# Performance work log

Measured on AMD Instinct MI355X. Metric: run time of the kernel, lower is better.

The kernel has to match this reference:

```python
import jax, jax.numpy as jnp
import numpy as np

B, Q, KL, ML, D = 2, 1024, 1024, 1024, 1024
H, DK = 16, 64  # adim = H*DK = 1024
SCALE = float(np.sqrt(DK))


def _rel_shift(x):
    # x: [B, qlen, klen, H] -> TransformerXL relative shift
    b, q, k, h = x.shape
    x = jnp.pad(x, ((0, 0), (0, 0), (1, 0), (0, 0)))  # [B,q,k+1,H]
    x = x.reshape(b, k + 1, q, h)[:, 1:]               # drop first row of shifted view
    return x.reshape(b, q, k, h)


def setup_inputs() -> dict:
    key = jax.random.key(0)
    ks = jax.random.split(key, 12)
    n = lambda i, s, scale=1.0: jax.random.normal(ks[i], s, jnp.float32) * scale
    return {
        "key_x": n(0, (B, KL, D)),
        "query": n(1, (B, Q, D)),
        "memory": n(2, (B, ML, D)),
        "pos_embs": n(3, (KL + ML, 1, D)),
        "mask": jnp.ones((B, Q, KL + ML), jnp.int32),
        "u": n(4, (H, DK), 0.02),
        "v": n(5, (H, DK), 0.02),
        "w_key": n(6, (D, H * DK), 0.02),
        "w_value": n(7, (D, H * DK), 0.02),
        "w_query": n(8, (D, H * DK), 0.02),
        "w_position": n(9, (D, H * DK), 0.02),
        "w_out": n(10, (H * DK, D), 0.02),
    }


def reference(key_x, query, memory, pos_embs, mask, u, v,
              w_key, w_value, w_query, w_position, w_out):
    bs, qlen = query.shape[:2]
    kv = jnp.concatenate([memory, key_x], axis=1)          # [B, mlen+klen, D]
    klen_tot = kv.shape[1]
    val = (kv @ w_value).reshape(bs, klen_tot, H, DK)
    k = (kv @ w_key).reshape(bs, klen_tot, H, DK)
    q = (query @ w_query).reshape(bs, qlen, H, DK)
    pos = (pos_embs.reshape(-1, pos_embs.shape[-1]) @ w_position).reshape(-1, H, DK)
    AC = jnp.einsum('bihd,bjhd->bijh', q + u[None, None], k)
    BD = jnp.einsum('bihd,jhd->bijh', q + v[None, None], pos)
    BD = _rel_shift(BD)
    e = (AC + BD) / SCALE                                   # [B, q, k, H]
    neg_inf = jnp.finfo(e.dtype).min
    e = jnp.where(mask[..., None] == 0, neg_inf, e)
    aw = jax.nn.softmax(e, axis=2)
    cv = jnp.einsum('bijh,bjhd->bihd', aw, val).reshape(bs, qlen, H * DK)
    cv = cv @ w_out
    return cv, aw.transpose(0, 3, 1, 2)
```

## Files before the change

### kernel.cpp

```cpp
#include <hip/hip_runtime.h>
#include <stdint.h>

#define H 16
#define DK 64
#define QL 1024
#define KT 2048
#define DM 1024
#define BATCH 2

typedef __attribute__((ext_vector_type(4))) float f32x4;
typedef __attribute__((ext_vector_type(8))) short s16x8;

enum { EPI_K = 0, EPI_V = 1, EPI_QUV = 2, EPI_P = 3, EPI_OUT = 4 };

__device__ __forceinline__ unsigned short f2bf(float f) {
  union { float f; uint32_t u; } v; v.f = f;
  uint32_t u = v.u;
  u += 0x7fffu + ((u >> 16) & 1u);
  return (unsigned short)(u >> 16);
}

#define MFMA_BF16(A, B, C) __builtin_amdgcn_mfma_f32_16x16x32_bf16((A), (B), (C), 0, 0, 0)

__device__ __forceinline__ void gld_lds16(const void* g, void* l) {
  __builtin_amdgcn_global_load_lds(
      (const __attribute__((address_space(1))) void*)g,
      (__attribute__((address_space(3))) void*)l, 16, 0, 0);
}

__device__ __forceinline__ void store_bf16_col(char* base, int g, int col2, const f32x4& v) {
  uint32_t pk01, pk23;
  asm("v_cvt_pk_bf16_f32 %0, %1, %2" : "=v"(pk01) : "v"(v[0]), "v"(v[1]));
  asm("v_cvt_pk_bf16_f32 %0, %1, %2" : "=v"(pk23) : "v"(v[2]), "v"(v[3]));
  const int rr = g * 4;
  *(uint16_t*)(base + (rr + 0) * 128 + (col2 ^ (((rr + 0) & 7) << 4))) = (uint16_t)pk01;
  *(uint16_t*)(base + (rr + 1) * 128 + (col2 ^ (((rr + 1) & 7) << 4))) = (uint16_t)(pk01 >> 16);
  *(uint16_t*)(base + (rr + 2) * 128 + (col2 ^ (((rr + 2) & 7) << 4))) = (uint16_t)pk23;
  *(uint16_t*)(base + (rr + 3) * 128 + (col2 ^ (((rr + 3) & 7) << 4))) = (uint16_t)(pk23 >> 16);
}


__global__ __launch_bounds__(256) void cast_kv_kernel(
    const float* __restrict__ mem, const float* __restrict__ keyx,
    unsigned short* __restrict__ kv) {
  size_t i4 = (size_t)blockIdx.x * blockDim.x + threadIdx.x;
  if (i4 >= (size_t)BATCH * KT * DM / 4) return;
  size_t e = i4 * 4;
  int b = (int)(e >> 21);
  int rem = (int)(e & ((1u << 21) - 1));
  int j = rem >> 10;
  int d = rem & 1023;
  const float* src = (j < 1024)
      ? (mem + ((size_t)b << 20) + ((size_t)j << 10) + d)
      : (keyx + ((size_t)b << 20) + ((size_t)(j - 1024) << 10) + d);
  float4 v = *(const float4*)src;
  ushort4 o;
  o.x = f2bf(v.x); o.y = f2bf(v.y); o.z = f2bf(v.z); o.w = f2bf(v.w);
  *(ushort4*)(kv + e) = o;
}

__global__ __launch_bounds__(256) void cast4_kernel(
    const float* __restrict__ src, unsigned short* __restrict__ dst, int n4) {
  int i4 = blockIdx.x * blockDim.x + threadIdx.x;
  if (i4 >= n4) return;
  float4 v = *(const float4*)(src + (size_t)i4 * 4);
  ushort4 o;
  o.x = f2bf(v.x); o.y = f2bf(v.y); o.z = f2bf(v.z); o.w = f2bf(v.w);
  *(ushort4*)(dst + (size_t)i4 * 4) = o;
}

__global__ __launch_bounds__(256) void transpose_cast_kernel(
    const float* __restrict__ w0, const float* __restrict__ w1,
    const float* __restrict__ w2, const float* __restrict__ w3,
    const float* __restrict__ w4,
    unsigned short* __restrict__ o0, unsigned short* __restrict__ o1,
    unsigned short* __restrict__ o2, unsigned short* __restrict__ o3,
    unsigned short* __restrict__ o4) {
  __shared__ float tile[32][33];
  const float* src; unsigned short* dst;
  switch (blockIdx.z) {
    case 0: src = w0; dst = o0; break;
    case 1: src = w1; dst = o1; break;
    case 2: src = w2; dst = o2; break;
    case 3: src = w3; dst = o3; break;
    default: src = w4; dst = o4; break;
  }
  int bx = blockIdx.x * 32, by = blockIdx.y * 32;
  int tx = threadIdx.x;
  int ty = threadIdx.y;
#pragma unroll
  for (int r = 0; r < 4; ++r)
    tile[ty + r * 8][tx] = src[(size_t)(by + ty + r * 8) * DM + bx + tx];
  __syncthreads();
#pragma unroll
  for (int r = 0; r < 4; ++r)
    dst[(size_t)(bx + ty + r * 8) * DM + by + tx] = f2bf(tile[tx][ty + r * 8]);
}

__global__ __launch_bounds__(256) void pack_mask_kernel(
    const int* __restrict__ mask, unsigned long long* __restrict__ bits) {
  int t = blockIdx.x * blockDim.x + threadIdx.x;
  int wid = t >> 6, lane = t & 63;
  int v = mask[(size_t)wid * 64 + lane];
  unsigned long long bb = __ballot(v != 0);
  if (lane == 0) bits[wid] = bb;
}


__device__ __forceinline__ void gemm_body(
    const unsigned short* __restrict__ A, const unsigned short* __restrict__ B,
    int mode,
    unsigned short* __restrict__ out0, unsigned short* __restrict__ out1,
    float* __restrict__ outf,
    const float* __restrict__ uvec, const float* __restrict__ vvec,
    int bx, int by) {
  __shared__ __align__(16) unsigned short lds[128 * 64 * 2];
  char* As = (char*)lds;
  char* Bs = (char*)lds + 128 * 64 * 2;

  const int tid = threadIdx.x;
  const int w = tid >> 6, lane = tid & 63;
  const int g = lane >> 4, l15 = lane & 15;
  const int m0 = by * 128, n0 = bx * 128;
  const int wm = w >> 1, wn = w & 1;
  const int K = 1024;

  f32x4 zf = {0.f, 0.f, 0.f, 0.f};
  f32x4 acc[4][4];
#pragma unroll
  for (int a = 0; a < 4; ++a)
#pragma unroll
    for (int c = 0; c < 4; ++c) acc[a][c] = zf;

  for (int kt = 0; kt < K; kt += 64) {
#pragma unroll
    for (int q = 0; q < 4; ++q) {
      int o = (w * 4 + q) * 1024 + lane * 16;
      int row = o >> 7;
      int slot = (o & 127) >> 4;
      int ks = slot ^ (row & 7);
      gld_lds16(A + (size_t)(m0 + row) * K + kt + ks * 8, As + o);
      gld_lds16(B + (size_t)(n0 + row) * K + kt + ks * 8, Bs + o);
    }
    asm volatile("s_waitcnt vmcnt(0)" ::: "memory");
    __syncthreads();
#pragma unroll
    for (int kk = 0; kk < 2; ++kk) {
      s16x8 af[4], bfr[4];
#pragma unroll
      for (int mf = 0; mf < 4; ++mf) {
        int row = wm * 64 + mf * 16 + l15;
        af[mf] = *(const s16x8*)(As + row * 128 + ((kk * 64 + g * 16) ^ ((row & 7) << 4)));
      }
#pragma unroll
      for (int nf = 0; nf < 4; ++nf) {
        int row = wn * 64 + nf * 16 + l15;
        bfr[nf] = *(const s16x8*)(Bs + row * 128 + ((kk * 64 + g * 16) ^ ((row & 7) << 4)));
      }
#pragma unroll
      for (int mf = 0; mf < 4; ++mf)
#pragma unroll
        for (int nf = 0; nf < 4; ++nf)
          acc[mf][nf] = MFMA_BF16(af[mf], bfr[nf], acc[mf][nf]);
    }
    __syncthreads();
  }

#pragma unroll
  for (int mf = 0; mf < 4; ++mf) {
#pragma unroll
    for (int nf = 0; nf < 4; ++nf) {
#pragma unroll
      for (int i = 0; i < 4; ++i) {
        int m = m0 + wm * 64 + mf * 16 + g * 4 + i;
        int n = n0 + wn * 64 + nf * 16 + l15;
        float val = acc[mf][nf][i];
        if (mode == EPI_K) {
          int b = m >> 11, j = m & 2047, hh = n >> 6, d = n & 63;
          out0[(((size_t)(b * H + hh) * KT + j) << 6) + d] = f2bf(val);
        } else if (mode == EPI_V) {
          int hh = m >> 6, d = m & 63, b = n >> 11, j = n & 2047;
          out0[((size_t)(b * H + hh) * 64 + d) * KT + j] = f2bf(val);
        } else if (mode == EPI_QUV) {
          int b = m >> 10, i2 = m & 1023, hh = n >> 6, d = n & 63;
          size_t idx = ((size_t)(b * H + hh) * QL + i2) * 64 + d;
          out0[idx] = f2bf(val + uvec[n]);
          out1[idx] = f2bf(val + vvec[n]);
        } else if (mode == EPI_P) {
          int hh = n >> 6, d = n & 63;
          out0[(((size_t)hh * KT + m) << 6) + d] = f2bf(val);
        } else {
          outf[(size_t)m * DM + n] = val;
        }
      }
    }
  }
}

__global__ __launch_bounds__(256) void gemm_fused_kernel(
    const unsigned short* __restrict__ kv, const unsigned short* __restrict__ q_b,
    const unsigned short* __restrict__ pos_b,
    const unsigned short* __restrict__ wk, const unsigned short* __restrict__ wv,
    const unsigned short* __restrict__ wq, const unsigned short* __restrict__ wp,
    unsigned short* __restrict__ Kp, unsigned short* __restrict__ Vt,
    unsigned short* __restrict__ Qu, unsigned short* __restrict__ Qv,
    unsigned short* __restrict__ Pp,
    const float* __restrict__ u, const float* __restrict__ v) {
  int bid = blockIdx.x;
  const unsigned short *A, *B;
  unsigned short *o0, *o1 = nullptr;
  int mode, bx, by;
  if (bid < 256)      { A = kv;    B = wk; mode = EPI_K;   o0 = Kp; bx = bid & 7;  by = bid >> 3; }
  else if (bid < 512) { bid -= 256; A = wv; B = kv; mode = EPI_V;   o0 = Vt; bx = bid & 31; by = bid >> 5; }
  else if (bid < 640) { bid -= 512; A = q_b; B = wq; mode = EPI_QUV; o0 = Qu; o1 = Qv; bx = bid & 7; by = bid >> 3; }
  else                { bid -= 640; A = pos_b; B = wp; mode = EPI_P; o0 = Pp; bx = bid & 7; by = bid >> 3; }
  gemm_body(A, B, mode, o0, o1, nullptr, u, v, bx, by);
}

__global__ __launch_bounds__(256) void gemm_out_kernel(
    const unsigned short* __restrict__ A, const unsigned short* __restrict__ B,
    float* __restrict__ outf) {
  gemm_body(A, B, EPI_OUT, nullptr, nullptr, outf, nullptr, nullptr, blockIdx.x, blockIdx.y);
}


__device__ __forceinline__ void bd_chunk(
    f32x4 (&out)[4], const unsigned short* __restrict__ Pp_b,
    const s16x8* qv, const s16x8* qvp, int tbase, int g, int l15) {
  const s16x8 zv = {0, 0, 0, 0, 0, 0, 0, 0};
  const f32x4 zf = {0.f, 0.f, 0.f, 0.f};
#pragma unroll
  for (int nf = 0; nf < 4; ++nf) {
    const int F0 = tbase + nf * 16;
    const bool wrap = (F0 >= KT);
    const int prow = (wrap ? F0 - (KT + 1) : F0) + l15;
    const s16x8* psrc = (const s16x8*)(Pp_b + (size_t)(prow < 0 ? 0 : prow) * 64 + g * 8);
    f32x4 c = zf;
#pragma unroll
    for (int kk = 0; kk < 2; ++kk) {
      s16x8 pb = psrc[kk * 4];
      if (prow < 0) pb = zv;
      c = MFMA_BF16(wrap ? qvp[kk] : qv[kk], pb, c);
    }
    out[nf] = c;
  }
}

__device__ __forceinline__ void bd_gather(
    float (&bd)[4][4], const f32x4 (&cur)[4], const f32x4& nxt0,
    const int (&slan)[4], const bool (&crr)[4]) {
#pragma unroll
  for (int i = 0; i < 4; ++i) {
    float s0 = __shfl(cur[0][i], slan[i]);
    float s1 = __shfl(cur[1][i], slan[i]);
    float s2 = __shfl(cur[2][i], slan[i]);
    float s3 = __shfl(cur[3][i], slan[i]);
    float s4 = __shfl(nxt0[i], slan[i]);
    bd[0][i] = crr[i] ? s1 : s0;
    bd[1][i] = crr[i] ? s2 : s1;
    bd[2][i] = crr[i] ? s3 : s2;
    bd[3][i] = crr[i] ? s4 : s3;
  }
}

__device__ __forceinline__ void load_k(
    s16x8 (&kb)[2][4], const unsigned short* __restrict__ Kp_b,
    int j0, int g, int l15) {
#pragma unroll
  for (int nf = 0; nf < 4; ++nf) {
    const s16x8* p = (const s16x8*)(Kp_b + (size_t)(j0 + nf * 16 + l15) * 64 + g * 8);
    kb[0][nf] = p[0];
    kb[1][nf] = p[4];
  }
}

__device__ __forceinline__ void load_v(
    s16x8 (&vb)[2][4], const unsigned short* __restrict__ Vt_b,
    int j0, int g, int l15) {
#pragma unroll
  for (int df = 0; df < 4; ++df) {
    const unsigned short* p = Vt_b + (size_t)(df * 16 + l15) * KT + j0 + g * 8;
    vb[0][df] = *(const s16x8*)(p);
    vb[1][df] = *(const s16x8*)(p + 32);
  }
}

__device__ __forceinline__ void qk_acc(
    f32x4 (&acc)[4], const s16x8* qu, const s16x8 (&kb)[2][4]) {
#pragma unroll
  for (int kk = 0; kk < 2; ++kk)
#pragma unroll
    for (int nf = 0; nf < 4; ++nf)
      acc[nf] = MFMA_BF16(qu[kk], kb[kk][nf], acc[nf]);
}

__device__ __forceinline__ void make_e(
    float (&e)[4][4], const f32x4 (&acc)[4], const float (&bd)[4][4],
    const unsigned long long* __restrict__ mb_b,
    int r0, int s, int g, int l15) {
#pragma unroll
  for (int i = 0; i < 4; ++i) {
    unsigned long long mw = mb_b[(size_t)(r0 + g * 4 + i) * 32 + s];
#pragma unroll
    for (int nf = 0; nf < 4; ++nf) {
      float ev = (acc[nf][i] + bd[nf][i]) * 0.125f;
      e[nf][i] = ((mw >> (nf * 16 + l15)) & 1ull) ? ev : -1e30f;
    }
  }
}

#define ATTN_DECODE()                                                  \
  const int w = threadIdx.x >> 6, lane = threadIdx.x & 63;             \
  const int g = lane >> 4, l15 = lane & 15;                            \
  const int logical = ((blockIdx.x & 7) << 9) | (blockIdx.x >> 3);     \
  const int rblk = logical & 15, jq = (logical >> 4) & 7, bh = logical >> 7; \
  const int b = bh >> 4, h = bh & 15;                                  \
  const int r0 = rblk * 64 + w * 16;                                   \
  (void)b; (void)h;

#define ATTN_PROLOGUE()                                                \
  s16x8 zv = {0, 0, 0, 0, 0, 0, 0, 0};                                 \
  s16x8 qu[2], qv[2], qvp[2];                                          \
  {                                                                    \
    int r = r0 + l15;                                                  \
    const s16x8* pq = (const s16x8*)(Qu_b + (size_t)r * 64 + g * 8);   \
    const s16x8* pv = (const s16x8*)(Qv_b + (size_t)r * 64 + g * 8);   \
    qu[0] = pq[0]; qu[1] = pq[4];                                      \
    qv[0] = pv[0]; qv[1] = pv[4];                                      \
    int rp = r0 + 1 + l15;                                             \
    if (rp < QL) {                                                     \
      const s16x8* pp = (const s16x8*)(Qv_b + (size_t)rp * 64 + g * 8);\
      qvp[0] = pp[0]; qvp[1] = pp[4];                                  \
    } else { qvp[0] = zv; qvp[1] = zv; }                               \
  }                                                                    \
  int slan[4]; bool crr[4];                                            \
  _Pragma("unroll")                                                    \
  for (int i = 0; i < 4; ++i) {                                        \
    int g4i = g * 4 + i;                                               \
    slan[i] = (lane & 48) | ((l15 + 15 - g4i) & 15);                   \
    crr[i] = (l15 >= g4i + 1);                                         \
  }                                                                    \
  const int sq0 = jq * 4;                                              \
  const int tb0 = sq0 * 64 + 1008 - r0;

__global__ __launch_bounds__(256) void attn_p1(
    const unsigned short* __restrict__ Qu, const unsigned short* __restrict__ Qv,
    const unsigned short* __restrict__ Kp, const unsigned short* __restrict__ Pp,
    const unsigned long long* __restrict__ mbits,
    float2* __restrict__ mlp, float* __restrict__ Oacc) {
  ATTN_DECODE();

  if (jq == 0) {
    float4 z4 = {0.f, 0.f, 0.f, 0.f};
    float* dst = Oacc + ((size_t)bh * QL + rblk * 64) * 64 + threadIdx.x * 16;
#pragma unroll
    for (int q = 0; q < 4; ++q) ((float4*)dst)[q] = z4;
  }

  const unsigned short* Qu_b = Qu + (size_t)bh * QL * 64;
  const unsigned short* Qv_b = Qv + (size_t)bh * QL * 64;
  const unsigned short* Kp_b = Kp + (size_t)bh * KT * 64;
  const unsigned short* Pp_b = Pp + (size_t)h * KT * 64;
  const unsigned long long* mb_b = mbits + (size_t)b * QL * 32;

  ATTN_PROLOGUE();

  float m_l[4], l_l[4];
#pragma unroll
  for (int i = 0; i < 4; ++i) { m_l[i] = -1e30f; l_l[i] = 0.f; }

  f32x4 cur[4], nxt[4];
  bd_chunk(cur, Pp_b, qv, qvp, tb0, g, l15);
  s16x8 kb[2][4];
  load_k(kb, Kp_b, sq0 * 64, g, l15);

#pragma unroll
  for (int ss = 0; ss < 4; ++ss) {
    const int s = sq0 + ss;
    bd_chunk(nxt, Pp_b, qv, qvp, tb0 + (ss + 1) * 64, g, l15);
    f32x4 acc[4];
#pragma unroll
    for (int nf = 0; nf < 4; ++nf) acc[nf] = f32x4{0.f, 0.f, 0.f, 0.f};
    qk_acc(acc, qu, kb);
    if (ss < 3) load_k(kb, Kp_b, (s + 1) * 64, g, l15);
    float bd[4][4];
    bd_gather(bd, cur, nxt[0], slan, crr);
    float e[4][4];
    make_e(e, acc, bd, mb_b, r0, s, g, l15);
#pragma unroll
    for (int i = 0; i < 4; ++i) {
      float tmax = fmaxf(fmaxf(e[0][i], e[1][i]), fmaxf(e[2][i], e[3][i]));
      float mnew = fmaxf(m_l[i], tmax);
      l_l[i] = l_l[i] * __expf(m_l[i] - mnew) + __expf(e[0][i] - mnew) +
               __expf(e[1][i] - mnew) + __expf(e[2][i] - mnew) + __expf(e[3][i] - mnew);
      m_l[i] = mnew;
    }
#pragma unroll
    for (int nf = 0; nf < 4; ++nf) cur[nf] = nxt[nf];
  }

#pragma unroll
  for (int i = 0; i < 4; ++i) {
    float m_r = m_l[i];
#pragma unroll
    for (int d = 1; d < 16; d <<= 1) m_r = fmaxf(m_r, __shfl_xor(m_r, d));
    float contrib = l_l[i] * __expf(m_l[i] - m_r);
#pragma unroll
    for (int d = 1; d < 16; d <<= 1) contrib += __shfl_xor(contrib, d);
    if (l15 == 0) {
      float2 p2; p2.x = m_r; p2.y = contrib;
      mlp[((size_t)bh * QL + r0 + g * 4 + i) * 8 + jq] = p2;
    }
  }
}

__global__ __launch_bounds__(256) void attn_p2(
    const unsigned short* __restrict__ Qu, const unsigned short* __restrict__ Qv,
    const unsigned short* __restrict__ Kp, const unsigned short* __restrict__ Vt,
    const unsigned short* __restrict__ Pp,
    const unsigned long long* __restrict__ mbits,
    const float2* __restrict__ mlp,
    float* __restrict__ aw, float* __restrict__ Oacc) {
  __shared__ __align__(16) unsigned short smem[8192];
  ATTN_DECODE();

  const unsigned short* Qu_b = Qu + (size_t)bh * QL * 64;
  const unsigned short* Qv_b = Qv + (size_t)bh * QL * 64;
  const unsigned short* Kp_b = Kp + (size_t)bh * KT * 64;
  const unsigned short* Vt_b = Vt + (size_t)bh * 64 * KT;
  const unsigned short* Pp_b = Pp + (size_t)h * KT * 64;
  float* aw_b = aw + (size_t)bh * QL * KT;
  const unsigned long long* mb_b = mbits + (size_t)b * QL * 32;
  char* pl0 = (char*)smem + w * 4096;
  char* pl1 = pl0 + 2048;

  float m_f = -1e30f, l_f = 0.f;
  {
    float2 mq[8];
#pragma unroll
    for (int q = 0; q < 8; ++q) mq[q] = mlp[((size_t)bh * QL + r0 + l15) * 8 + q];
#pragma unroll
    for (int q = 0; q < 8; ++q) m_f = fmaxf(m_f, mq[q].x);
#pragma unroll
    for (int q = 0; q < 8; ++q) l_f += mq[q].y * __expf(mq[q].x - m_f);
  }
  float rl = 1.f / l_f;
  float m_fi[4], rl_i[4];
#pragma unroll
  for (int i = 0; i < 4; ++i) {
    m_fi[i] = __shfl(m_f, g * 4 + i);
    rl_i[i] = __shfl(rl, g * 4 + i);
  }

  ATTN_PROLOGUE();

  f32x4 accO[4];
#pragma unroll
  for (int df = 0; df < 4; ++df) accO[df] = f32x4{0.f, 0.f, 0.f, 0.f};

  f32x4 cur[4], nxt[4];
  bd_chunk(cur, Pp_b, qv, qvp, tb0, g, l15);
  s16x8 kb[2][4], vb[2][4];
  load_k(kb, Kp_b, sq0 * 64, g, l15);

#pragma unroll
  for (int ss = 0; ss < 4; ++ss) {
    const int s = sq0 + ss;
    const int j0 = s * 64;
    bd_chunk(nxt, Pp_b, qv, qvp, tb0 + (ss + 1) * 64, g, l15);
    f32x4 acc[4];
#pragma unroll
    for (int nf = 0; nf < 4; ++nf) acc[nf] = f32x4{0.f, 0.f, 0.f, 0.f};
    qk_acc(acc, qu, kb);
    if (ss < 3) load_k(kb, Kp_b, j0 + 64, g, l15);
    float bd[4][4];
    bd_gather(bd, cur, nxt[0], slan, crr);
    float e[4][4];
    make_e(e, acc, bd, mb_b, r0, s, g, l15);

    if (ss > 0) {
      char* prd = (ss & 1) ? pl0 : pl1;
#pragma unroll
      for (int kk = 0; kk < 2; ++kk) {
        s16x8 pa = *(const s16x8*)(prd + l15 * 128 + ((kk * 64 + g * 16) ^ ((l15 & 7) << 4)));
#pragma unroll
        for (int df = 0; df < 4; ++df)
          accO[df] = MFMA_BF16(pa, vb[kk][df], accO[df]);
      }
    }
    load_v(vb, Vt_b, j0, g, l15);

    char* pwr = (ss & 1) ? pl1 : pl0;
#pragma unroll
    for (int nf = 0; nf < 4; ++nf) {
      f32x4 pv4;
#pragma unroll
      for (int i = 0; i < 4; ++i) {
        float p = __expf(e[nf][i] - m_fi[i]) * rl_i[i];
        aw_b[(size_t)(r0 + g * 4 + i) * KT + j0 + nf * 16 + l15] = p;
        pv4[i] = p;
      }
      store_bf16_col(pwr, g, (nf * 16 + l15) * 2, pv4);
    }
#pragma unroll
    for (int nf = 0; nf < 4; ++nf) cur[nf] = nxt[nf];
  }

  {
#pragma unroll
    for (int kk = 0; kk < 2; ++kk) {
      s16x8 pa = *(const s16x8*)(pl1 + l15 * 128 + ((kk * 64 + g * 16) ^ ((l15 & 7) << 4)));
#pragma unroll
      for (int df = 0; df < 4; ++df)
        accO[df] = MFMA_BF16(pa, vb[kk][df], accO[df]);
    }
  }

#pragma unroll
  for (int df = 0; df < 4; ++df)
#pragma unroll
    for (int i = 0; i < 4; ++i)
      atomicAdd(&Oacc[((size_t)bh * QL + r0 + g * 4 + i) * 64 + df * 16 + l15], accO[df][i]);
}

__global__ __launch_bounds__(256) void cast_cv_kernel(
    const float* __restrict__ Oacc, unsigned short* __restrict__ cvb) {
  int t = blockIdx.x * blockDim.x + threadIdx.x;
  int d4 = t & 15, r = (t >> 4) & 1023, bh = t >> 14;
  int b = bh >> 4, h = bh & 15;
  float4 v = ((const float4*)Oacc)[t];
  ushort4 o;
  o.x = f2bf(v.x); o.y = f2bf(v.y); o.z = f2bf(v.z); o.w = f2bf(v.w);
  *(ushort4*)(cvb + (size_t)(b * QL + r) * DM + h * 64 + d4 * 4) = o;
}


extern "C" void kernel_launch(void* const* d_in, const int* in_sizes, int n_in,
                              void* d_out, int out_size, void* d_ws, size_t ws_size,
                              hipStream_t stream) {
  const float* key_x  = (const float*)d_in[0];
  const float* query  = (const float*)d_in[1];
  const float* memory = (const float*)d_in[2];
  const float* pose   = (const float*)d_in[3];
  const int*   mask   = (const int*)d_in[4];
  const float* u      = (const float*)d_in[5];
  const float* v      = (const float*)d_in[6];
  const float* w_key  = (const float*)d_in[7];
  const float* w_val  = (const float*)d_in[8];
  const float* w_qry  = (const float*)d_in[9];
  const float* w_pos  = (const float*)d_in[10];
  const float* w_out  = (const float*)d_in[11];

  char* ws = (char*)d_ws;
  const size_t MB = 1024 * 1024;
  unsigned short* kv_b  = (unsigned short*)(ws + 0);
  unsigned short* q_b   = (unsigned short*)(ws + 8 * MB);
  unsigned short* pos_b = (unsigned short*)(ws + 12 * MB);
  unsigned short* wk_t  = (unsigned short*)(ws + 16 * MB);
  unsigned short* wv_t  = (unsigned short*)(ws + 18 * MB);
  unsigned short* wq_t  = (unsigned short*)(ws + 20 * MB);
  unsigned short* wp_t  = (unsigned short*)(ws + 22 * MB);
  unsigned short* wo_t  = (unsigned short*)(ws + 24 * MB);
  unsigned short* Kp    = (unsigned short*)(ws + 26 * MB);
  unsigned short* Vt    = (unsigned short*)(ws + 34 * MB);
  unsigned short* Qu    = (unsigned short*)(ws + 42 * MB);
  unsigned short* Qv    = (unsigned short*)(ws + 46 * MB);
  unsigned short* Pp    = (unsigned short*)(ws + 50 * MB);
  unsigned short* cvb   = (unsigned short*)(ws + 54 * MB);
  unsigned long long* mb = (unsigned long long*)(ws + 58 * MB);
  float*  Oacc = (float*)(ws + 0);
  float2* mlp  = (float2*)(ws + 8 * MB);

  float* out_cv = (float*)d_out;
  float* out_aw = (float*)d_out + (size_t)BATCH * QL * DM;

  cast_kv_kernel<<<4096, 256, 0, stream>>>(memory, key_x, kv_b);
  cast4_kernel<<<2048, 256, 0, stream>>>(query, q_b, BATCH * QL * DM / 4);
  cast4_kernel<<<2048, 256, 0, stream>>>(pose, pos_b, KT * DM / 4);
  transpose_cast_kernel<<<dim3(32, 32, 5), dim3(32, 8), 0, stream>>>(
      w_key, w_val, w_qry, w_pos, w_out, wk_t, wv_t, wq_t, wp_t, wo_t);
  pack_mask_kernel<<<16384, 256, 0, stream>>>(mask, mb);

  gemm_fused_kernel<<<768, 256, 0, stream>>>(kv_b, q_b, pos_b, wk_t, wv_t, wq_t, wp_t,
                                             Kp, Vt, Qu, Qv, Pp, u, v);

  attn_p1<<<4096, 256, 0, stream>>>(Qu, Qv, Kp, Pp, mb, mlp, Oacc);
  attn_p2<<<4096, 256, 0, stream>>>(Qu, Qv, Kp, Vt, Pp, mb, mlp, out_aw, Oacc);
  cast_cv_kernel<<<2048, 256, 0, stream>>>(Oacc, cvb);

  gemm_out_kernel<<<dim3(8, 16), 256, 0, stream>>>(cvb, wo_t, out_cv);
}
```

Baseline: 483.7 us.

## Store unnormalized softmax in pass one and normalize during a PV-only pass

The first attention pass now computes exp(e) directly, with no running-max subtraction, writes it into the attention-weight output, and records per-chunk row sums. A small kernel turns those sums into reciprocals. A new PV kernel then reads the stored weights back, rescales them in place, converts them to bf16 and runs the PV MFMAs. This removes the second recomputation of the QK and relative-position (BD) scores and the LDS staging. In exchange it adds a full extra read and write of the large fp32 attention-weight tensor. Dropping the max subtraction also risks exp overflow when logits are large.

Measured after the change: 481.5 us. Within noise of the previous version (-0.5%).

```diff
diff --git a/kernel.cpp b/kernel.cpp
--- a/kernel.cpp
+++ b/kernel.cpp
@@ -28,15 +28,13 @@
       (__attribute__((address_space(3))) void*)l, 16, 0, 0);
 }
 
-__device__ __forceinline__ void store_bf16_col(char* base, int g, int col2, const f32x4& v) {
-  uint32_t pk01, pk23;
-  asm("v_cvt_pk_bf16_f32 %0, %1, %2" : "=v"(pk01) : "v"(v[0]), "v"(v[1]));
-  asm("v_cvt_pk_bf16_f32 %0, %1, %2" : "=v"(pk23) : "v"(v[2]), "v"(v[3]));
-  const int rr = g * 4;
-  *(uint16_t*)(base + (rr + 0) * 128 + (col2 ^ (((rr + 0) & 7) << 4))) = (uint16_t)pk01;
-  *(uint16_t*)(base + (rr + 1) * 128 + (col2 ^ (((rr + 1) & 7) << 4))) = (uint16_t)(pk01 >> 16);
-  *(uint16_t*)(base + (rr + 2) * 128 + (col2 ^ (((rr + 2) & 7) << 4))) = (uint16_t)pk23;
-  *(uint16_t*)(base + (rr + 3) * 128 + (col2 ^ (((rr + 3) & 7) << 4))) = (uint16_t)(pk23 >> 16);
+__device__ __forceinline__ s16x8 cvt8(const f32x4& a, const f32x4& b) {
+  union { uint32_t u[4]; s16x8 v; } r;
+  asm("v_cvt_pk_bf16_f32 %0, %1, %2" : "=v"(r.u[0]) : "v"(a[0]), "v"(a[1]));
+  asm("v_cvt_pk_bf16_f32 %0, %1, %2" : "=v"(r.u[1]) : "v"(a[2]), "v"(a[3]));
+  asm("v_cvt_pk_bf16_f32 %0, %1, %2" : "=v"(r.u[2]) : "v"(b[0]), "v"(b[1]));
+  asm("v_cvt_pk_bf16_f32 %0, %1, %2" : "=v"(r.u[3]) : "v"(b[2]), "v"(b[3]));
+  return r.v;
 }
 
 
@@ -316,7 +314,7 @@
   const int rblk = logical & 15, jq = (logical >> 4) & 7, bh = logical >> 7; \
   const int b = bh >> 4, h = bh & 15;                                  \
   const int r0 = rblk * 64 + w * 16;                                   \
-  (void)b; (void)h;
+  (void)b; (void)h; (void)lane;
 
 #define ATTN_PROLOGUE()                                                \
   s16x8 zv = {0, 0, 0, 0, 0, 0, 0, 0};                                 \
@@ -347,7 +345,7 @@
     const unsigned short* __restrict__ Qu, const unsigned short* __restrict__ Qv,
     const unsigned short* __restrict__ Kp, const unsigned short* __restrict__ Pp,
     const unsigned long long* __restrict__ mbits,
-    float2* __restrict__ mlp, float* __restrict__ Oacc) {
+    float* __restrict__ aw, float* __restrict__ lsum, float* __restrict__ Oacc) {
   ATTN_DECODE();
 
   if (jq == 0) {
@@ -361,13 +359,12 @@
   const unsigned short* Qv_b = Qv + (size_t)bh * QL * 64;
   const unsigned short* Kp_b = Kp + (size_t)bh * KT * 64;
   const unsigned short* Pp_b = Pp + (size_t)h * KT * 64;
+  float* aw_b = aw + (size_t)bh * QL * KT;
   const unsigned long long* mb_b = mbits + (size_t)b * QL * 32;
 
   ATTN_PROLOGUE();
 
-  float m_l[4], l_l[4];
-#pragma unroll
-  for (int i = 0; i < 4; ++i) { m_l[i] = -1e30f; l_l[i] = 0.f; }
+  float l_l[4] = {0.f, 0.f, 0.f, 0.f};
 
   f32x4 cur[4], nxt[4];
   bd_chunk(cur, Pp_b, qv, qvp, tb0, g, l15);
@@ -377,6 +374,7 @@
 #pragma unroll
   for (int ss = 0; ss < 4; ++ss) {
     const int s = sq0 + ss;
+    const int j0 = s * 64;
     bd_chunk(nxt, Pp_b, qv, qvp, tb0 + (ss + 1) * 64, g, l15);
     f32x4 acc[4];
 #pragma unroll
@@ -388,131 +386,70 @@
     float e[4][4];
     make_e(e, acc, bd, mb_b, r0, s, g, l15);
 #pragma unroll
-    for (int i = 0; i < 4; ++i) {
-      float tmax = fmaxf(fmaxf(e[0][i], e[1][i]), fmaxf(e[2][i], e[3][i]));
-      float mnew = fmaxf(m_l[i], tmax);
-      l_l[i] = l_l[i] * __expf(m_l[i] - mnew) + __expf(e[0][i] - mnew) +
-               __expf(e[1][i] - mnew) + __expf(e[2][i] - mnew) + __expf(e[3][i] - mnew);
-      m_l[i] = mnew;
-    }
+    for (int nf = 0; nf < 4; ++nf)
+#pragma unroll
+      for (int i = 0; i < 4; ++i) {
+        float p = __expf(e[nf][i]);
+        aw_b[(size_t)(r0 + g * 4 + i) * KT + j0 + nf * 16 + l15] = p;
+        l_l[i] += p;
+      }
 #pragma unroll
     for (int nf = 0; nf < 4; ++nf) cur[nf] = nxt[nf];
   }
 
 #pragma unroll
   for (int i = 0; i < 4; ++i) {
-    float m_r = m_l[i];
-#pragma unroll
-    for (int d = 1; d < 16; d <<= 1) m_r = fmaxf(m_r, __shfl_xor(m_r, d));
-    float contrib = l_l[i] * __expf(m_l[i] - m_r);
-#pragma unroll
-    for (int d = 1; d < 16; d <<= 1) contrib += __shfl_xor(contrib, d);
-    if (l15 == 0) {
-      float2 p2; p2.x = m_r; p2.y = contrib;
-      mlp[((size_t)bh * QL + r0 + g * 4 + i) * 8 + jq] = p2;
-    }
-  }
-}
-
-__global__ __launch_bounds__(256) void attn_p2(
-    const unsigned short* __restrict__ Qu, const unsigned short* __restrict__ Qv,
-    const unsigned short* __restrict__ Kp, const unsigned short* __restrict__ Vt,
-    const unsigned short* __restrict__ Pp,
-    const unsigned long long* __restrict__ mbits,
-    const float2* __restrict__ mlp,
+    float sL = l_l[i];
+#pragma unroll
+    for (int d = 1; d < 16; d <<= 1) sL += __shfl_xor(sL, d);
+    if (l15 == 0)
+      lsum[((size_t)bh * QL + r0 + g * 4 + i) * 8 + jq] = sL;
+  }
+}
+
+__global__ __launch_bounds__(256) void rsum_kernel(
+    const float* __restrict__ lsum, float* __restrict__ rl) {
+  int r = blockIdx.x * 256 + threadIdx.x;
+  const f32x4* p = (const f32x4*)(lsum + (size_t)r * 8);
+  f32x4 a = p[0], c = p[1];
+  rl[r] = 1.f / (a[0] + a[1] + a[2] + a[3] + c[0] + c[1] + c[2] + c[3]);
+}
+
+__global__ __launch_bounds__(256) void attn_pv(
+    const unsigned short* __restrict__ Vt, const float* __restrict__ rl,
     float* __restrict__ aw, float* __restrict__ Oacc) {
-  __shared__ __align__(16) unsigned short smem[8192];
   ATTN_DECODE();
 
-  const unsigned short* Qu_b = Qu + (size_t)bh * QL * 64;
-  const unsigned short* Qv_b = Qv + (size_t)bh * QL * 64;
-  const unsigned short* Kp_b = Kp + (size_t)bh * KT * 64;
   const unsigned short* Vt_b = Vt + (size_t)bh * 64 * KT;
-  const unsigned short* Pp_b = Pp + (size_t)h * KT * 64;
   float* aw_b = aw + (size_t)bh * QL * KT;
-  const unsigned long long* mb_b = mbits + (size_t)b * QL * 32;
-  char* pl0 = (char*)smem + w * 4096;
-  char* pl1 = pl0 + 2048;
-
-  float m_f = -1e30f, l_f = 0.f;
-  {
-    float2 mq[8];
-#pragma unroll
-    for (int q = 0; q < 8; ++q) mq[q] = mlp[((size_t)bh * QL + r0 + l15) * 8 + q];
-#pragma unroll
-    for (int q = 0; q < 8; ++q) m_f = fmaxf(m_f, mq[q].x);
-#pragma unroll
-    for (int q = 0; q < 8; ++q) l_f += mq[q].y * __expf(mq[q].x - m_f);
-  }
-  float rl = 1.f / l_f;
-  float m_fi[4], rl_i[4];
-#pragma unroll
-  for (int i = 0; i < 4; ++i) {
-    m_fi[i] = __shfl(m_f, g * 4 + i);
-    rl_i[i] = __shfl(rl, g * 4 + i);
-  }
-
-  ATTN_PROLOGUE();
+  const int sq0 = jq * 4;
+  const float rs = rl[(size_t)bh * QL + r0 + l15];
 
   f32x4 accO[4];
 #pragma unroll
   for (int df = 0; df < 4; ++df) accO[df] = f32x4{0.f, 0.f, 0.f, 0.f};
 
-  f32x4 cur[4], nxt[4];
-  bd_chunk(cur, Pp_b, qv, qvp, tb0, g, l15);
-  s16x8 kb[2][4], vb[2][4];
-  load_k(kb, Kp_b, sq0 * 64, g, l15);
-
 #pragma unroll
   for (int ss = 0; ss < 4; ++ss) {
-    const int s = sq0 + ss;
-    const int j0 = s * 64;
-    bd_chunk(nxt, Pp_b, qv, qvp, tb0 + (ss + 1) * 64, g, l15);
-    f32x4 acc[4];
-#pragma unroll
-    for (int nf = 0; nf < 4; ++nf) acc[nf] = f32x4{0.f, 0.f, 0.f, 0.f};
-    qk_acc(acc, qu, kb);
-    if (ss < 3) load_k(kb, Kp_b, j0 + 64, g, l15);
-    float bd[4][4];
-    bd_gather(bd, cur, nxt[0], slan, crr);
-    float e[4][4];
-    make_e(e, acc, bd, mb_b, r0, s, g, l15);
-
-    if (ss > 0) {
-      char* prd = (ss & 1) ? pl0 : pl1;
-#pragma unroll
-      for (int kk = 0; kk < 2; ++kk) {
-        s16x8 pa = *(const s16x8*)(prd + l15 * 128 + ((kk * 64 + g * 16) ^ ((l15 & 7) << 4)));
-#pragma unroll
-        for (int df = 0; df < 4; ++df)
-          accO[df] = MFMA_BF16(pa, vb[kk][df], accO[df]);
-      }
-    }
+    const int j0 = (sq0 + ss) * 64;
+    float* ar = aw_b + (size_t)(r0 + l15) * KT + j0 + g * 8;
+    f32x4 w0 = *(const f32x4*)(ar);
+    f32x4 w1 = *(const f32x4*)(ar + 4);
+    f32x4 w2 = *(const f32x4*)(ar + 32);
+    f32x4 w3 = *(const f32x4*)(ar + 36);
+    w0 *= rs; w1 *= rs; w2 *= rs; w3 *= rs;
+    *(f32x4*)(ar) = w0;
+    *(f32x4*)(ar + 4) = w1;
+    *(f32x4*)(ar + 32) = w2;
+    *(f32x4*)(ar + 36) = w3;
+    s16x8 pa0 = cvt8(w0, w1);
+    s16x8 pa1 = cvt8(w2, w3);
+    s16x8 vb[2][4];
     load_v(vb, Vt_b, j0, g, l15);
-
-    char* pwr = (ss & 1) ? pl1 : pl0;
-#pragma unroll
-    for (int nf = 0; nf < 4; ++nf) {
-      f32x4 pv4;
-#pragma unroll
-      for (int i = 0; i < 4; ++i) {
-        float p = __expf(e[nf][i] - m_fi[i]) * rl_i[i];
-        aw_b[(size_t)(r0 + g * 4 + i) * KT + j0 + nf * 16 + l15] = p;
-        pv4[i] = p;
-      }
-      store_bf16_col(pwr, g, (nf * 16 + l15) * 2, pv4);
-    }
-#pragma unroll
-    for (int nf = 0; nf < 4; ++nf) cur[nf] = nxt[nf];
-  }
-
-  {
-#pragma unroll
-    for (int kk = 0; kk < 2; ++kk) {
-      s16x8 pa = *(const s16x8*)(pl1 + l15 * 128 + ((kk * 64 + g * 16) ^ ((l15 & 7) << 4)));
-#pragma unroll
-      for (int df = 0; df < 4; ++df)
-        accO[df] = MFMA_BF16(pa, vb[kk][df], accO[df]);
+#pragma unroll
+    for (int df = 0; df < 4; ++df) {
+      accO[df] = MFMA_BF16(pa0, vb[0][df], accO[df]);
+      accO[df] = MFMA_BF16(pa1, vb[1][df], accO[df]);
     }
   }
 
@@ -568,8 +505,9 @@
   unsigned short* Pp    = (unsigned short*)(ws + 50 * MB);
   unsigned short* cvb   = (unsigned short*)(ws + 54 * MB);
   unsigned long long* mb = (unsigned long long*)(ws + 58 * MB);
-  float*  Oacc = (float*)(ws + 0);
-  float2* mlp  = (float2*)(ws + 8 * MB);
+  float* Oacc = (float*)(ws + 0);
+  float* lsum = (float*)(ws + 8 * MB);
+  float* rl   = (float*)(ws + 9 * MB);
 
   float* out_cv = (float*)d_out;
   float* out_aw = (float*)d_out + (size_t)BATCH * QL * DM;
@@ -584,8 +522,9 @@
   gemm_fused_kernel<<<768, 256, 0, stream>>>(kv_b, q_b, pos_b, wk_t, wv_t, wq_t, wp_t,
                                              Kp, Vt, Qu, Qv, Pp, u, v);
 
-  attn_p1<<<4096, 256, 0, stream>>>(Qu, Qv, Kp, Pp, mb, mlp, Oacc);
-  attn_p2<<<4096, 256, 0, stream>>>(Qu, Qv, Kp, Vt, Pp, mb, mlp, out_aw, Oacc);
+  attn_p1<<<4096, 256, 0, stream>>>(Qu, Qv, Kp, Pp, mb, out_aw, lsum, Oacc);
+  rsum_kernel<<<128, 256, 0, stream>>>(lsum, rl);
+  attn_pv<<<4096, 256, 0, stream>>>(Vt, rl, out_aw, Oacc);
   cast_cv_kernel<<<2048, 256, 0, stream>>>(Oacc, cvb);
 
   gemm_out_kernel<<<dim3(8, 16), 256, 0, stream>>>(cvb, wo_t, out_cv);
```
